# Optimization experiments

Hardware: AMD Instinct MI355X
Metric: run time of the kernel (lower is better)

Reference implementation:

```python
import jax, jax.numpy as jnp
import numpy as np

N_WIRES = 4
N_LAYERS = 2
BSZ = 4096


def _gate(p):
    # combined single-qubit gate RX(p2) @ RZ(p1) @ RY(p0)  (RY applied first)
    a, b, c = p[0] * 0.5, p[1] * 0.5, p[2] * 0.5
    ca, sa = jnp.cos(a), jnp.sin(a)
    ry = jnp.stack([jnp.stack([ca, -sa]), jnp.stack([sa, ca])]).astype(jnp.complex64)
    eb = (jnp.cos(b) - 1j * jnp.sin(b)).astype(jnp.complex64)  # e^{-i b}
    zero = jnp.zeros((), jnp.complex64)
    rz = jnp.stack([jnp.stack([eb, zero]), jnp.stack([zero, jnp.conj(eb)])])
    cc, sc = jnp.cos(c), jnp.sin(c)
    rx = jnp.stack([jnp.stack([cc + 0j, -1j * sc]), jnp.stack([-1j * sc, cc + 0j])]).astype(jnp.complex64)
    return rx @ rz @ ry


def _apply1(state, U, w):
    # state: (N,2,2,2,2); apply 2x2 gate U on wire w
    s = jnp.moveaxis(state, w + 1, 4)
    s = jnp.einsum('nijka,ba->nijkb', s, U)
    return jnp.moveaxis(s, 4, w + 1)


def _cnot(state, c, t):
    s = jnp.moveaxis(state, (c + 1, t + 1), (1, 2))
    s = jnp.stack([s[:, 0], jnp.flip(s[:, 1], axis=1)], axis=1)
    return jnp.moveaxis(s, (1, 2), (c + 1, t + 1))


def _quanv(x, params):
    bsz = x.shape[0]
    # extract 2x2 patches in the same order as the torch loop:
    # [x[r,c], x[r,c+1], x[r+1,c], x[r+1,c+1]], row-major over (r,c)
    p = x.reshape(bsz, 14, 2, 14, 2).transpose(0, 1, 3, 2, 4).reshape(bsz * 196, 4)
    h = p * 0.5
    v = jnp.stack([jnp.cos(h), jnp.sin(h)], axis=-1).astype(jnp.complex64)  # (N,4,2): RY(patch)|0>
    state = jnp.einsum('na,nb,nc,nd->nabcd', v[:, 0], v[:, 1], v[:, 2], v[:, 3])
    for l in range(N_LAYERS):
        for w in range(N_WIRES):
            state = _apply1(state, _gate(params[l, w]), w)
        for w in range(N_WIRES - 1):
            state = _cnot(state, w, w + 1)
        state = _cnot(state, N_WIRES - 1, 0)
    probs = state.real ** 2 + state.imag ** 2  # (N,2,2,2,2)
    z = jnp.array([1.0, -1.0], jnp.float32)
    exps = []
    for w in range(N_WIRES):
        axes = tuple(i for i in range(1, 5) if i != w + 1)
        exps.append(probs.sum(axes) @ z)  # <Z_w>, shape (N,)
    # (N,4) -> (bsz, 196, 4) -> (bsz, 784), patch-major / wire-minor like torch.cat
    return jnp.stack(exps, axis=-1).reshape(bsz, 196 * N_WIRES)


def setup_inputs() -> dict:
    key = jax.random.key(0)
    k1, k2 = jax.random.split(key)
    x = jax.random.uniform(k1, (BSZ, 28, 28), dtype=jnp.float32)
    params = jax.random.normal(k2, (N_LAYERS, N_WIRES, 3), dtype=jnp.float32)
    return {"x": x, "params": params}


def reference(x, params):
    return _quanv(x, params)
```

## Files before the change

kernel.cpp:

```cpp
#include <hip/hip_runtime.h>


typedef _Float16 f16;
typedef _Float16 half8 __attribute__((ext_vector_type(8)));
typedef float f4 __attribute__((ext_vector_type(4)));

__device__ __forceinline__ float2 cmulf(float2 a, float2 b) {
    return make_float2(fmaf(a.x, b.x, -(a.y * b.y)),
                       fmaf(a.x, b.y,   a.y * b.x));
}

#define PK2(a, b) __builtin_bit_cast(float, __builtin_amdgcn_cvt_pkrtz((a), (b)))

__global__ __launch_bounds__(256, 4) void quanv_kernel(
        const float* __restrict__ x,
        const float* __restrict__ params,
        float* __restrict__ out)
{
    __shared__ float4 Gs[8];
    __shared__ __align__(16) f16 Wt[32][40];
    __shared__ __align__(16) unsigned char SB[4][5120];

    const int t = threadIdx.x;

    if (t < 8) {
        const float* p = params + t * 3;
        const float a = 0.5f * p[0], b = 0.5f * p[1], c = 0.5f * p[2];
        const float sa = __sinf(a), ca = __cosf(a);
        const float sb = __sinf(b), cb = __cosf(b);
        const float sc = __sinf(c), cc = __cosf(c);
        const float ax = cc*ca*cb + sc*sa*sb;
        const float ay = -(cc*ca*sb + sc*sa*cb);
        const float bx = sc*ca*sb - cc*sa*cb;
        const float by = cc*sa*sb - sc*ca*cb;
        Gs[t] = make_float4(ax, ay, bx, by);
    }
    __syncthreads();

    {
        const unsigned long long IDX1P = 0x497a2f1c85b6e3d0ULL;
        const unsigned long long INV1P = 0xa3185ce7d46f2b90ULL;
        const int i = t >> 4;
        const int m = t & 15;
        const int j = (int)((IDX1P >> (i * 4)) & 15);
        const int k = (int)((INV1P >> (m * 4)) & 15);
        float2 e = make_float2(1.f, 0.f);
#pragma unroll
        for (int w = 0; w < 4; ++w) {
            const float4 g = Gs[4 + w];
            const int jb = (j >> (3 - w)) & 1;
            const int kb = (k >> (3 - w)) & 1;
            const float ux = jb ? (kb ?  g.x : -g.z) : (kb ? g.z : g.x);
            const float uy = jb ? (kb ? -g.y :  g.w) : (kb ? g.w : g.y);
            e = cmulf(e, make_float2(ux, uy));
        }
        Wt[i][m]           = (f16)e.x;
        Wt[i][16 + m]      = (f16)(-e.y);
        Wt[16 + i][m]      = (f16)e.y;
        Wt[16 + i][16 + m] = (f16)e.x;
    }

    const int gid = blockIdx.x * 256 + t;
    const int n = gid / 196;
    const int p = gid - n * 196;
    const int r = p / 14;
    const int c = p - r * 14;

    const float* xb = x + n * 784 + r * 56 + c * 2;
    const float2 top = *(const float2*)(xb);
    const float2 bot = *(const float2*)(xb + 28);

    float pw[4] = {0.5f * top.x, 0.5f * top.y, 0.5f * bot.x, 0.5f * bot.y};
    float2 wv[4][2];
#pragma unroll
    for (int w = 0; w < 4; ++w) {
        const float cw = __cosf(pw[w]);
        const float sw = __sinf(pw[w]);
        const float4 g = Gs[w];
        wv[w][0] = make_float2(fmaf(g.z, sw, g.x * cw),  fmaf(g.w, sw, g.y * cw));
        wv[w][1] = make_float2(fmaf(g.x, sw, -g.z * cw), fmaf(-g.y, sw, g.w * cw));
    }

    float2 ab[4], cd[4];
#pragma unroll
    for (int i = 0; i < 2; ++i)
#pragma unroll
        for (int j = 0; j < 2; ++j) {
            ab[i * 2 + j] = cmulf(wv[0][i], wv[1][j]);
            cd[i * 2 + j] = cmulf(wv[2][i], wv[3][j]);
        }
    float2 s[16];
#pragma unroll
    for (int hi = 0; hi < 4; ++hi)
#pragma unroll
        for (int lo = 0; lo < 4; ++lo)
            s[hi * 4 + lo] = cmulf(ab[hi], cd[lo]);

    const int l   = t & 63;
    const int wid = t >> 6;
    const int q   = l >> 4;
    const int c16 = l & 15;

    f16* st = (f16*)(SB[wid] + l * 80);
    const float4 r0 = make_float4(PK2(s[0].x, s[1].x),  PK2(s[2].x, s[3].x),
                                  PK2(s[4].x, s[5].x),  PK2(s[6].x, s[7].x));
    const float4 r1 = make_float4(PK2(s[8].x, s[9].x),  PK2(s[10].x, s[11].x),
                                  PK2(s[12].x, s[13].x), PK2(s[14].x, s[15].x));
    const float4 r2 = make_float4(PK2(s[0].y, s[1].y),  PK2(s[2].y, s[3].y),
                                  PK2(s[4].y, s[5].y),  PK2(s[6].y, s[7].y));
    const float4 r3 = make_float4(PK2(s[8].y, s[9].y),  PK2(s[10].y, s[11].y),
                                  PK2(s[12].y, s[13].y), PK2(s[14].y, s[15].y));
    *(float4*)(st)      = r0;
    *(float4*)(st + 8)  = r1;
    *(float4*)(st + 16) = r2;
    *(float4*)(st + 24) = r3;

    __syncthreads();

    const half8 b0 = *(const half8*)&Wt[c16][q * 8];
    const half8 b1 = *(const half8*)&Wt[16 + c16][q * 8];
    const f4 zf4 = {0.f, 0.f, 0.f, 0.f};
    f4 d0[4], d1[4];
#pragma unroll
    for (int m = 0; m < 4; ++m) {
        const half8 am = *(const half8*)((const f16*)(SB[wid] + (m * 16 + c16) * 80) + q * 8);
        d0[m] = __builtin_amdgcn_mfma_f32_16x16x32_f16(am, b0, zf4, 0, 0, 0);
        d1[m] = __builtin_amdgcn_mfma_f32_16x16x32_f16(am, b1, zf4, 0, 0, 0);
    }

    float* prb = (float*)SB[wid];
#pragma unroll
    for (int m = 0; m < 4; ++m)
#pragma unroll
        for (int reg = 0; reg < 4; ++reg) {
            const float pv = fmaf(d0[m][reg], d0[m][reg], d1[m][reg] * d1[m][reg]);
            prb[(m * 16 + q * 4 + reg) * 20 + c16] = pv;
        }

    const float4 p0 = *(const float4*)(prb + l * 20);
    const float4 p1 = *(const float4*)(prb + l * 20 + 4);
    const float4 p2 = *(const float4*)(prb + l * 20 + 8);
    const float4 p3 = *(const float4*)(prb + l * 20 + 12);

    const float t00 = p0.x + p0.y + p0.z + p0.w;
    const float t01 = p1.x + p1.y + p1.z + p1.w;
    const float t10 = p2.x + p2.y + p2.z + p2.w;
    const float t11 = p3.x + p3.y + p3.z + p3.w;
    const float e0 = (t00 + t01) - (t10 + t11);
    const float e1 = (t00 - t01) + (t10 - t11);

    const float u00 = p0.x + p1.x + p2.x + p3.x;
    const float u01 = p0.y + p1.y + p2.y + p3.y;
    const float u10 = p0.z + p1.z + p2.z + p3.z;
    const float u11 = p0.w + p1.w + p2.w + p3.w;
    const float e2 = (u00 + u01) - (u10 + u11);
    const float e3 = (u00 - u01) + (u10 - u11);

    *(float4*)(out + gid * 4) = make_float4(e0, e1, e2, e3);
}

extern "C" void kernel_launch(void* const* d_in, const int* in_sizes, int n_in,
                              void* d_out, int out_size, void* d_ws, size_t ws_size,
                              hipStream_t stream) {
    const float* x      = (const float*)d_in[0];
    const float* params = (const float*)d_in[1];
    float* out = (float*)d_out;

    const int npatch = 4096 * 196;
    quanv_kernel<<<npatch / 256, 256, 0, stream>>>(x, params, out);
}
```

Measured before the change: 71.84 us.

## Use single-wave blocks with readlane-broadcast gate parameters and interleaved complex layout

Shrinks blocks from 256 to 64 threads so each block is one wavefront. Gate coefficients are computed per lane and broadcast with readlane rather than staged in shared memory behind a barrier. Each wave now builds the full unitary matrix itself, and the state is stored as interleaved real/imag fp16 pairs. The intent is to drop a block-wide barrier and cross-wave coupling, at the cost of recomputing the gate and unitary setup four times as often and launching four times as many blocks.

New measurement: 76.57 us. 1.07x slower.

```diff
diff --git a/kernel.cpp b/kernel.cpp
--- a/kernel.cpp
+++ b/kernel.cpp
@@ -5,80 +5,80 @@
 typedef _Float16 half8 __attribute__((ext_vector_type(8)));
 typedef float f4 __attribute__((ext_vector_type(4)));
 
+#define PK2(a, b) __builtin_bit_cast(float, __builtin_amdgcn_cvt_pkrtz((a), (b)))
+#define RDL(x, g) __builtin_bit_cast(float, __builtin_amdgcn_readlane(__builtin_bit_cast(int, (x)), (g)))
+
 __device__ __forceinline__ float2 cmulf(float2 a, float2 b) {
     return make_float2(fmaf(a.x, b.x, -(a.y * b.y)),
                        fmaf(a.x, b.y,   a.y * b.x));
 }
 
-#define PK2(a, b) __builtin_bit_cast(float, __builtin_amdgcn_cvt_pkrtz((a), (b)))
-
-__global__ __launch_bounds__(256, 4) void quanv_kernel(
+__global__ __launch_bounds__(64, 4) void quanv_kernel(
         const float* __restrict__ x,
         const float* __restrict__ params,
         float* __restrict__ out)
 {
-    __shared__ float4 Gs[8];
     __shared__ __align__(16) f16 Wt[32][40];
-    __shared__ __align__(16) unsigned char SB[4][5120];
+    __shared__ __align__(16) unsigned char SB[64 * 80];
 
-    const int t = threadIdx.x;
+    const int l = threadIdx.x;
+    const int gid = blockIdx.x * 64 + l;
 
-    if (t < 8) {
-        const float* p = params + t * 3;
-        const float a = 0.5f * p[0], b = 0.5f * p[1], c = 0.5f * p[2];
-        const float sa = __sinf(a), ca = __cosf(a);
-        const float sb = __sinf(b), cb = __cosf(b);
-        const float sc = __sinf(c), cc = __cosf(c);
-        const float ax = cc*ca*cb + sc*sa*sb;
-        const float ay = -(cc*ca*sb + sc*sa*cb);
-        const float bx = sc*ca*sb - cc*sa*cb;
-        const float by = cc*sa*sb - sc*ca*cb;
-        Gs[t] = make_float4(ax, ay, bx, by);
-    }
-    __syncthreads();
-
-    {
-        const unsigned long long IDX1P = 0x497a2f1c85b6e3d0ULL;
-        const unsigned long long INV1P = 0xa3185ce7d46f2b90ULL;
-        const int i = t >> 4;
-        const int m = t & 15;
-        const int j = (int)((IDX1P >> (i * 4)) & 15);
-        const int k = (int)((INV1P >> (m * 4)) & 15);
-        float2 e = make_float2(1.f, 0.f);
-#pragma unroll
-        for (int w = 0; w < 4; ++w) {
-            const float4 g = Gs[4 + w];
-            const int jb = (j >> (3 - w)) & 1;
-            const int kb = (k >> (3 - w)) & 1;
-            const float ux = jb ? (kb ?  g.x : -g.z) : (kb ? g.z : g.x);
-            const float uy = jb ? (kb ? -g.y :  g.w) : (kb ? g.w : g.y);
-            e = cmulf(e, make_float2(ux, uy));
-        }
-        Wt[i][m]           = (f16)e.x;
-        Wt[i][16 + m]      = (f16)(-e.y);
-        Wt[16 + i][m]      = (f16)e.y;
-        Wt[16 + i][16 + m] = (f16)e.x;
-    }
-
-    const int gid = blockIdx.x * 256 + t;
     const int n = gid / 196;
     const int p = gid - n * 196;
     const int r = p / 14;
     const int c = p - r * 14;
-
     const float* xb = x + n * 784 + r * 56 + c * 2;
     const float2 top = *(const float2*)(xb);
     const float2 bot = *(const float2*)(xb + 28);
 
-    float pw[4] = {0.5f * top.x, 0.5f * top.y, 0.5f * bot.x, 0.5f * bot.y};
+    const float* pg = params + (l & 7) * 3;
+    const float ha = 0.5f * pg[0], hb = 0.5f * pg[1], hc = 0.5f * pg[2];
+    const float sa = __sinf(ha), ca = __cosf(ha);
+    const float sb = __sinf(hb), cb = __cosf(hb);
+    const float sc = __sinf(hc), cx = __cosf(hc);
+    const float gx = cx*ca*cb + sc*sa*sb;
+    const float gy = -(cx*ca*sb + sc*sa*cb);
+    const float gz = sc*ca*sb - cx*sa*cb;
+    const float gw = cx*sa*sb - sc*ca*cb;
+    float Ax[8], Ay[8], Bx[8], By[8];
+#pragma unroll
+    for (int g = 0; g < 8; ++g) {
+        Ax[g] = RDL(gx, g); Ay[g] = RDL(gy, g);
+        Bx[g] = RDL(gz, g); By[g] = RDL(gw, g);
+    }
+
+    const unsigned long long IDX1P = 0x497a2f1c85b6e3d0ULL;
+    const unsigned long long INV1P = 0xa3185ce7d46f2b90ULL;
+    const int mE = l & 15;
+    const int kN = (int)((INV1P >> (mE * 4)) & 15);
+#pragma unroll
+    for (int ii = 0; ii < 4; ++ii) {
+        const int iE = (l >> 4) + 4 * ii;
+        const int jN = (int)((IDX1P >> (iE * 4)) & 15);
+        float2 e = make_float2(1.f, 0.f);
+#pragma unroll
+        for (int w = 0; w < 4; ++w) {
+            const int jb = (jN >> (3 - w)) & 1;
+            const int kb = (kN >> (3 - w)) & 1;
+            const float ux = jb ? (kb ?  Ax[4+w] : -Bx[4+w]) : (kb ? Bx[4+w] : Ax[4+w]);
+            const float uy = jb ? (kb ? -Ay[4+w] :  By[4+w]) : (kb ? By[4+w] : Ay[4+w]);
+            e = cmulf(e, make_float2(ux, uy));
+        }
+        *(float*)&Wt[iE][2 * mE]      = PK2(e.x, -e.y);
+        *(float*)&Wt[16 + iE][2 * mE] = PK2(e.y,  e.x);
+    }
+
+    const float pw0 = 0.5f * top.x, pw1 = 0.5f * top.y;
+    const float pw2 = 0.5f * bot.x, pw3 = 0.5f * bot.y;
+    const float pwv[4] = {pw0, pw1, pw2, pw3};
     float2 wv[4][2];
 #pragma unroll
     for (int w = 0; w < 4; ++w) {
-        const float cw = __cosf(pw[w]);
-        const float sw = __sinf(pw[w]);
-        const float4 g = Gs[w];
-        wv[w][0] = make_float2(fmaf(g.z, sw, g.x * cw),  fmaf(g.w, sw, g.y * cw));
-        wv[w][1] = make_float2(fmaf(g.x, sw, -g.z * cw), fmaf(-g.y, sw, g.w * cw));
+        const float cw = __cosf(pwv[w]);
+        const float sw = __sinf(pwv[w]);
+        wv[w][0] = make_float2(fmaf(Bx[w], sw,  Ax[w] * cw), fmaf( By[w], sw, Ay[w] * cw));
+        wv[w][1] = make_float2(fmaf(Ax[w], sw, -Bx[w] * cw), fmaf(-Ay[w], sw, By[w] * cw));
     }
 
     float2 ab[4], cd[4];
@@ -89,46 +89,36 @@
             ab[i * 2 + j] = cmulf(wv[0][i], wv[1][j]);
             cd[i * 2 + j] = cmulf(wv[2][i], wv[3][j]);
         }
-    float2 s[16];
+    float sd[16];
 #pragma unroll
     for (int hi = 0; hi < 4; ++hi)
 #pragma unroll
-        for (int lo = 0; lo < 4; ++lo)
-            s[hi * 4 + lo] = cmulf(ab[hi], cd[lo]);
+        for (int lo = 0; lo < 4; ++lo) {
+            const float2 sv = cmulf(ab[hi], cd[lo]);
+            sd[hi * 4 + lo] = PK2(sv.x, sv.y);
+        }
 
-    const int l   = t & 63;
-    const int wid = t >> 6;
-    const int q   = l >> 4;
-    const int c16 = l & 15;
-
-    f16* st = (f16*)(SB[wid] + l * 80);
-    const float4 r0 = make_float4(PK2(s[0].x, s[1].x),  PK2(s[2].x, s[3].x),
-                                  PK2(s[4].x, s[5].x),  PK2(s[6].x, s[7].x));
-    const float4 r1 = make_float4(PK2(s[8].x, s[9].x),  PK2(s[10].x, s[11].x),
-                                  PK2(s[12].x, s[13].x), PK2(s[14].x, s[15].x));
-    const float4 r2 = make_float4(PK2(s[0].y, s[1].y),  PK2(s[2].y, s[3].y),
-                                  PK2(s[4].y, s[5].y),  PK2(s[6].y, s[7].y));
-    const float4 r3 = make_float4(PK2(s[8].y, s[9].y),  PK2(s[10].y, s[11].y),
-                                  PK2(s[12].y, s[13].y), PK2(s[14].y, s[15].y));
-    *(float4*)(st)      = r0;
-    *(float4*)(st + 8)  = r1;
-    *(float4*)(st + 16) = r2;
-    *(float4*)(st + 24) = r3;
+    f16* st = (f16*)(SB + l * 80);
+    *(float4*)(st)      = make_float4(sd[0],  sd[1],  sd[2],  sd[3]);
+    *(float4*)(st + 8)  = make_float4(sd[4],  sd[5],  sd[6],  sd[7]);
+    *(float4*)(st + 16) = make_float4(sd[8],  sd[9],  sd[10], sd[11]);
+    *(float4*)(st + 24) = make_float4(sd[12], sd[13], sd[14], sd[15]);
 
     __syncthreads();
 
+    const int q = l >> 4, c16 = l & 15;
     const half8 b0 = *(const half8*)&Wt[c16][q * 8];
     const half8 b1 = *(const half8*)&Wt[16 + c16][q * 8];
     const f4 zf4 = {0.f, 0.f, 0.f, 0.f};
     f4 d0[4], d1[4];
 #pragma unroll
     for (int m = 0; m < 4; ++m) {
-        const half8 am = *(const half8*)((const f16*)(SB[wid] + (m * 16 + c16) * 80) + q * 8);
+        const half8 am = *(const half8*)(SB + (m * 16 + c16) * 80 + q * 16);
         d0[m] = __builtin_amdgcn_mfma_f32_16x16x32_f16(am, b0, zf4, 0, 0, 0);
         d1[m] = __builtin_amdgcn_mfma_f32_16x16x32_f16(am, b1, zf4, 0, 0, 0);
     }
 
-    float* prb = (float*)SB[wid];
+    float* prb = (float*)SB;
 #pragma unroll
     for (int m = 0; m < 4; ++m)
 #pragma unroll
@@ -167,5 +157,5 @@
     float* out = (float*)d_out;
 
     const int npatch = 4096 * 196;
-    quanv_kernel<<<npatch / 256, 256, 0, stream>>>(x, params, out);
+    quanv_kernel<<<npatch / 64, 64, 0, stream>>>(x, params, out);
 }
```
